# Performance work log

Hardware: AMD Instinct MI355X
Metric: run time of the kernel (lower is better)

Reference implementation:

```python
import jax, jax.numpy as jnp
import numpy as np

N_SRC, N_DST, E = 10000, 10000, 640000
S, T, O, H = 128, 128, 128, 4
D = O // H


def setup_inputs() -> dict:
    key = jax.random.key(0)
    ks = jax.random.split(key, 12)
    f = lambda k, shape, fan: jax.random.normal(k, shape, dtype=jnp.float32) / np.float32(np.sqrt(fan))
    return {
        "x_src": jax.random.normal(ks[0], (N_SRC, S), dtype=jnp.float32),
        "x_dst": jax.random.normal(ks[1], (N_DST, T), dtype=jnp.float32),
        "W_pred1": f(ks[2], (S, T), T),
        "b_pred1": jnp.zeros((S,), jnp.float32),
        "W_pred2": f(ks[3], (S, S), S),
        "b_pred2": jnp.zeros((S,), jnp.float32),
        "W_res": f(ks[4], (H * D, S), S),
        "W_src": f(ks[5], (H * D, S), S),
        "W_dst": f(ks[6], (H * D, T), T),
        "att_src": jax.random.normal(ks[7], (1, H, D), dtype=jnp.float32) * 0.01,
        "att_dst": jax.random.normal(ks[8], (1, H, D), dtype=jnp.float32) * 0.01,
        "W_self": f(ks[9], (H * D, T), T),
        "b_self": jnp.zeros((H * D,), jnp.float32),
        "edge_src": jax.random.randint(ks[10], (E,), 0, N_SRC),
        "edge_dst": jax.random.randint(ks[11], (E,), 0, N_DST),
        "num_dst": N_DST,
    }


def reference(x_src, x_dst, W_pred1, b_pred1, W_pred2, b_pred2, W_res, W_src, W_dst,
              att_src, att_dst, W_self, b_self, edge_src, edge_dst, num_dst):
    h, d = att_src.shape[1], att_src.shape[2]
    # residual prediction path: pred_mlp(x_dst) = Lin2(ReLU(Lin1(x_dst)))
    pred = jax.nn.relu(x_dst @ W_pred1.T + b_pred1) @ W_pred2.T + b_pred2  # [Ndst,S]
    residual = x_src[edge_src] - pred[edge_dst]                            # [E,S]
    # per-node attention logits (equivalent to gather-then-dot, cheaper)
    a_s = ((x_src @ W_src.T).reshape(-1, h, d) * att_src).sum(-1)          # [Nsrc,H]
    a_d = ((x_dst @ W_dst.T).reshape(-1, h, d) * att_dst).sum(-1)          # [Ndst,H]
    alpha = jax.nn.leaky_relu(a_s[edge_src] + a_d[edge_dst], 0.2)          # [E,H]
    # edge softmax over incoming edges of each destination node
    amax = jax.ops.segment_max(alpha, edge_dst, num_segments=num_dst)      # [Ndst,H]
    ex = jnp.exp(alpha - amax[edge_dst])
    denom = jax.ops.segment_sum(ex, edge_dst, num_segments=num_dst)
    alpha = ex / (denom[edge_dst] + 1e-16)                                 # [E,H]
    # attention-weighted aggregation of transformed residuals
    msg = (residual @ W_res.T).reshape(-1, h, d) * alpha[:, :, None]       # [E,H,D]
    agg = jax.ops.segment_sum(msg.reshape(-1, h * d), edge_dst, num_segments=num_dst)
    return agg + x_dst @ W_self.T + b_self                                 # [Ndst,H*D]
```

## Files before the change

### kernel.cpp

```cpp
#include <hip/hip_runtime.h>

#define LEAKY 0.2f
#define CAP 160
#define CAPB 8192
#define CHUNK 2048

#define FMA4(A, S, V) do { (A).x += (S)*(V).x; (A).y += (S)*(V).y; (A).z += (S)*(V).z; (A).w += (S)*(V).w; } while (0)

struct GemmJob { const float* X; const float* W; const float* B; float* Y; int M; int relu; };

__device__ __forceinline__ void gemm128_block(
    const float* __restrict__ X, const float* __restrict__ W,
    const float* __restrict__ B, float* __restrict__ Y,
    int M, int relu, int row0,
    float* __restrict__ XsT , float* __restrict__ WTs ) {
  if (row0 >= M) return;
  const int tid = threadIdx.x;
  const int tx = tid & 15;
  const int ty = tid >> 4;
  float4 acc[8][2];
#pragma unroll
  for (int i = 0; i < 8; i++) {
    acc[i][0] = make_float4(0.f, 0.f, 0.f, 0.f);
    acc[i][1] = make_float4(0.f, 0.f, 0.f, 0.f);
  }
  const int rS = tid >> 1;
  const int kb = (tid & 1) * 16;

  for (int k0 = 0; k0 < 128; k0 += 32) {
    int rr = row0 + rS; if (rr >= M) rr = M - 1;
    const float* xp = X + (size_t)rr * 128 + k0 + kb;
    float4 a0 = *(const float4*)xp;
    float4 a1 = *(const float4*)(xp + 4);
    float4 a2 = *(const float4*)(xp + 8);
    float4 a3 = *(const float4*)(xp + 12);
    XsT[(kb + 0) * 128 + rS] = a0.x; XsT[(kb + 1) * 128 + rS] = a0.y;
    XsT[(kb + 2) * 128 + rS] = a0.z; XsT[(kb + 3) * 128 + rS] = a0.w;
    XsT[(kb + 4) * 128 + rS] = a1.x; XsT[(kb + 5) * 128 + rS] = a1.y;
    XsT[(kb + 6) * 128 + rS] = a1.z; XsT[(kb + 7) * 128 + rS] = a1.w;
    XsT[(kb + 8) * 128 + rS] = a2.x; XsT[(kb + 9) * 128 + rS] = a2.y;
    XsT[(kb +10) * 128 + rS] = a2.z; XsT[(kb +11) * 128 + rS] = a2.w;
    XsT[(kb +12) * 128 + rS] = a3.x; XsT[(kb +13) * 128 + rS] = a3.y;
    XsT[(kb +14) * 128 + rS] = a3.z; XsT[(kb +15) * 128 + rS] = a3.w;

    const float* wp = W + (size_t)rS * 128 + k0 + kb;
    float4 b0 = *(const float4*)wp;
    float4 b1 = *(const float4*)(wp + 4);
    float4 b2 = *(const float4*)(wp + 8);
    float4 b3 = *(const float4*)(wp + 12);
    WTs[(kb + 0) * 128 + rS] = b0.x; WTs[(kb + 1) * 128 + rS] = b0.y;
    WTs[(kb + 2) * 128 + rS] = b0.z; WTs[(kb + 3) * 128 + rS] = b0.w;
    WTs[(kb + 4) * 128 + rS] = b1.x; WTs[(kb + 5) * 128 + rS] = b1.y;
    WTs[(kb + 6) * 128 + rS] = b1.z; WTs[(kb + 7) * 128 + rS] = b1.w;
    WTs[(kb + 8) * 128 + rS] = b2.x; WTs[(kb + 9) * 128 + rS] = b2.y;
    WTs[(kb +10) * 128 + rS] = b2.z; WTs[(kb +11) * 128 + rS] = b2.w;
    WTs[(kb +12) * 128 + rS] = b3.x; WTs[(kb +13) * 128 + rS] = b3.y;
    WTs[(kb +14) * 128 + rS] = b3.z; WTs[(kb +15) * 128 + rS] = b3.w;
    __syncthreads();

#pragma unroll
    for (int k = 0; k < 32; k++) {
      float4 xa = *(const float4*)&XsT[k * 128 + ty * 4];
      float4 xb = *(const float4*)&XsT[k * 128 + 64 + ty * 4];
      float4 w0 = *(const float4*)&WTs[k * 128 + tx * 4];
      float4 w1 = *(const float4*)&WTs[k * 128 + 64 + tx * 4];
      FMA4(acc[0][0], xa.x, w0); FMA4(acc[0][1], xa.x, w1);
      FMA4(acc[1][0], xa.y, w0); FMA4(acc[1][1], xa.y, w1);
      FMA4(acc[2][0], xa.z, w0); FMA4(acc[2][1], xa.z, w1);
      FMA4(acc[3][0], xa.w, w0); FMA4(acc[3][1], xa.w, w1);
      FMA4(acc[4][0], xb.x, w0); FMA4(acc[4][1], xb.x, w1);
      FMA4(acc[5][0], xb.y, w0); FMA4(acc[5][1], xb.y, w1);
      FMA4(acc[6][0], xb.z, w0); FMA4(acc[6][1], xb.z, w1);
      FMA4(acc[7][0], xb.w, w0); FMA4(acc[7][1], xb.w, w1);
    }
    __syncthreads();
  }

  float4 bv0 = make_float4(0.f, 0.f, 0.f, 0.f);
  float4 bv1 = make_float4(0.f, 0.f, 0.f, 0.f);
  if (B) { bv0 = *(const float4*)(B + tx * 4); bv1 = *(const float4*)(B + 64 + tx * 4); }
#pragma unroll
  for (int i = 0; i < 8; i++) {
    int r = row0 + (i < 4 ? ty * 4 + i : 64 + ty * 4 + (i - 4));
    if (r < M) {
      float4 o0, o1;
      o0.x = acc[i][0].x + bv0.x; o0.y = acc[i][0].y + bv0.y;
      o0.z = acc[i][0].z + bv0.z; o0.w = acc[i][0].w + bv0.w;
      o1.x = acc[i][1].x + bv1.x; o1.y = acc[i][1].y + bv1.y;
      o1.z = acc[i][1].z + bv1.z; o1.w = acc[i][1].w + bv1.w;
      if (relu) {
        o0.x = fmaxf(o0.x, 0.f); o0.y = fmaxf(o0.y, 0.f);
        o0.z = fmaxf(o0.z, 0.f); o0.w = fmaxf(o0.w, 0.f);
        o1.x = fmaxf(o1.x, 0.f); o1.y = fmaxf(o1.y, 0.f);
        o1.z = fmaxf(o1.z, 0.f); o1.w = fmaxf(o1.w, 0.f);
      }
      *(float4*)(Y + (size_t)r * 128 + tx * 4) = o0;
      *(float4*)(Y + (size_t)r * 128 + 64 + tx * 4) = o1;
    }
  }
}

__device__ __forceinline__ void attn32_block(const float* __restrict__ X,
                                             const float* __restrict__ v,
                                             float* __restrict__ a, int M, int blk,
                                             float* __restrict__ vsf ) {
  int tid = threadIdx.x;
  for (int i = tid; i < 512; i += 256) vsf[i + ((i >> 5) << 2)] = v[i];
  __syncthreads();
  int g = tid >> 3, l = tid & 7;
  int n = blk * 32 + g;
  if (n >= M) return;
  const float* xp = X + (size_t)n * 128 + l * 16;
  float4 x0 = *(const float4*)xp;
  float4 x1 = *(const float4*)(xp + 4);
  float4 x2 = *(const float4*)(xp + 8);
  float4 x3 = *(const float4*)(xp + 12);
  const float4* vv = (const float4*)vsf;
  int s = l * 18;
  float4 p = make_float4(0.f, 0.f, 0.f, 0.f);
  FMA4(p, x0.x, vv[s + 0]); FMA4(p, x0.y, vv[s + 1]); FMA4(p, x0.z, vv[s + 2]); FMA4(p, x0.w, vv[s + 3]);
  FMA4(p, x1.x, vv[s + 4]); FMA4(p, x1.y, vv[s + 5]); FMA4(p, x1.z, vv[s + 6]); FMA4(p, x1.w, vv[s + 7]);
  FMA4(p, x2.x, vv[s + 9]); FMA4(p, x2.y, vv[s +10]); FMA4(p, x2.z, vv[s +11]); FMA4(p, x2.w, vv[s +12]);
  FMA4(p, x3.x, vv[s +13]); FMA4(p, x3.y, vv[s +14]); FMA4(p, x3.z, vv[s +15]); FMA4(p, x3.w, vv[s +16]);
#pragma unroll
  for (int off = 1; off < 8; off <<= 1) {
    p.x += __shfl_xor(p.x, off, 64);
    p.y += __shfl_xor(p.y, off, 64);
    p.z += __shfl_xor(p.z, off, 64);
    p.w += __shfl_xor(p.w, off, 64);
  }
  if (l == 0) *(float4*)(a + (size_t)n * 4) = p;
}

__global__ __launch_bounds__(256) void phase1(
    const float* __restrict__ Wsrc, const float* __restrict__ attsrc,
    const float* __restrict__ Wdst, const float* __restrict__ attdst,
    const float* __restrict__ W_res, const float* __restrict__ W2,
    const float* __restrict__ b2,
    GemmJob jA,
    float* __restrict__ v_src, float* __restrict__ v_dst,
    float* __restrict__ Wc, float* __restrict__ bc,
    const int* __restrict__ edge_src, const int* __restrict__ edge_dst,
    int* __restrict__ gcnt, int* __restrict__ bin,
    int E, int Nd, int NB, int GA, int Q1, int T1) {
  __shared__ float smem[8192];
  int bx = blockIdx.x, tid = threadIdx.x;
  int u = (bx & 7) * Q1 + (bx >> 3);
  if (u >= T1) return;
  if (u == 0) {
    int which = tid >> 7, k = tid & 127;
    const float* W = which ? Wdst : Wsrc;
    const float* att = which ? attdst : attsrc;
    float* v = which ? v_dst : v_src;
    float s[4] = {0.f, 0.f, 0.f, 0.f};
#pragma unroll
    for (int h = 0; h < 4; h++)
      for (int d = 0; d < 32; d++)
        s[h] += W[(size_t)(h * 32 + d) * 128 + k] * att[h * 32 + d];
#pragma unroll
    for (int h = 0; h < 4; h++) v[k * 4 + h] = s[h];
  } else if (u == 1) {
    if (tid < 128) {
      float s = 0.f;
      for (int i = 0; i < 128; i++) s += W_res[(size_t)tid * 128 + i] * b2[i];
      bc[tid] = s;
    }
  } else if (u < 66) {
    int id = (u - 2) * 256 + tid;
    int o = id >> 7, j = id & 127;
    float s = 0.f;
    for (int i = 0; i < 128; i++) s += W_res[(size_t)o * 128 + i] * W2[(size_t)i * 128 + j];
    Wc[(size_t)o * 128 + j] = s;
  } else if (u < 66 + GA) {
    gemm128_block(jA.X, jA.W, jA.B, jA.Y, jA.M, jA.relu, (u - 66) * 128, smem, smem + 4096);
  } else {
    int* pk    = (int*)smem;
    int* hist  = (int*)smem + CHUNK;
    int* gbase = hist + 160;
    int* lcur  = gbase + 160;
    int e0 = (u - 66 - GA) * CHUNK;
    int n = E - e0; if (n > CHUNK) n = CHUNK;
    if (n <= 0) return;
    for (int i = tid; i < NB; i += 256) hist[i] = 0;
    __syncthreads();
    for (int i = tid; i < n; i += 256) {
      int s = edge_src[e0 + i], d = edge_dst[e0 + i];
      pk[i] = (s << 14) | d;
      atomicAdd(&hist[d >> 6], 1);
    }
    __syncthreads();
    for (int b = tid; b < NB; b += 256) {
      gbase[b] = hist[b] ? atomicAdd(&gcnt[b], hist[b]) : 0;
      lcur[b] = 0;
    }
    __syncthreads();
    for (int i = tid; i < n; i += 256) {
      int p = pk[i];
      int b = (p & 16383) >> 6;
      int off = gbase[b] + atomicAdd(&lcur[b], 1);
      if (off < CAPB) bin[(size_t)b * CAPB + off] = p;
    }
  }
}

__global__ __launch_bounds__(256) void phase2(
    GemmJob j0, GemmJob j1, GemmJob j2,
    const float* __restrict__ x_src, const float* __restrict__ x_dst,
    const float* __restrict__ v_src, const float* __restrict__ v_dst,
    float* __restrict__ a_s, float* __restrict__ a_d,
    const int* __restrict__ gcnt, const int* __restrict__ bin,
    int* __restrict__ sorted_src, int* __restrict__ rstart, int* __restrict__ rend,
    int Ns, int Nd, int NB, int G, int As, int Ad, int Q2, int T2) {
  __shared__ float smem[8192];
  int bx = blockIdx.x, tid = threadIdx.x;
  int u = (bx % 6) * Q2 + bx / 6;
  if (u >= T2) return;
  if (u < 3 * G) {
    GemmJob J = (u < G) ? j0 : (u < 2 * G) ? j1 : j2;
    gemm128_block(J.X, J.W, J.B, J.Y, J.M, J.relu, (u % G) * 128, smem, smem + 4096);
  } else if (u < 3 * G + As) {
    attn32_block(x_src, v_src, a_s, Ns, u - 3 * G, smem);
  } else if (u < 3 * G + As + Ad) {
    attn32_block(x_dst, v_dst, a_d, Nd, u - 3 * G - As, smem);
  } else {
    int b = u - (3 * G + As + Ad);
    int* hist2 = (int*)smem;
    int* lcur2 = (int*)smem + 64;
    int cnt = gcnt[b]; if (cnt > CAPB) cnt = CAPB;
    size_t base = (size_t)b * CAPB;
    if (tid < 64) hist2[tid] = 0;
    __syncthreads();
    for (int i = tid; i < cnt; i += 256) atomicAdd(&hist2[bin[base + i] & 63], 1);
    __syncthreads();
    if (tid < 64) {
      int v = hist2[tid];
      int incl = v;
#pragma unroll
      for (int off = 1; off < 64; off <<= 1) {
        int t = __shfl_up(incl, off, 64);
        if (tid >= off) incl += t;
      }
      int st = incl - v;
      lcur2[tid] = st;
      int dst = (b << 6) + tid;
      if (dst < Nd) {
        rstart[dst] = (int)base + st;
        rend[dst]   = (int)base + st + v;
      }
    }
    __syncthreads();
    for (int i = tid; i < cnt; i += 256) {
      int p = bin[base + i];
      int j = p & 63;
      int lp = atomicAdd(&lcur2[j], 1);
      sorted_src[base + lp] = p >> 14;
    }
  }
}

__global__ __launch_bounds__(256) void phase3(
    const int* __restrict__ rstart, const int* __restrict__ rend,
    const int* __restrict__ sorted_src,
    const float* __restrict__ a_s, const float* __restrict__ a_d,
    const float* __restrict__ u_src, const float* __restrict__ u_pred,
    const float* __restrict__ self_o, float* __restrict__ out, int Nd) {
  __shared__ float smem[1920];
  int bx = blockIdx.x, tid = threadIdx.x;
  int half = tid >> 7;
  int t = tid & 127;
  int dst = bx * 2 + half;
  if (dst >= Nd) return;

  float* wbuf  = smem + half * 640;
  int* srcbuf  = (int*)(smem + 1280) + half * 160;
  float4* red4 = (float4*)(smem + 1600);
  float4* redv = (float4*)(smem + 1616) + half * 32;
  float* inv_s = smem + 1872 + half * 4;
  float* sA_s  = smem + 1880 + half * 4;

  int start = rstart[dst];
  int deg = rend[dst] - start;
  float4 ad4 = *(const float4*)(a_d + (size_t)dst * 4);
  float s0 = 0.f, s1 = 0.f, s2 = 0.f, s3 = 0.f;
  for (int i = t; i < deg; i += 128) {
    int src = sorted_src[start + i];
    float4 as4 = *(const float4*)(a_s + (size_t)src * 4);
    float l0 = as4.x + ad4.x; l0 = l0 > 0.f ? l0 : LEAKY * l0;
    float l1 = as4.y + ad4.y; l1 = l1 > 0.f ? l1 : LEAKY * l1;
    float l2 = as4.z + ad4.z; l2 = l2 > 0.f ? l2 : LEAKY * l2;
    float l3 = as4.w + ad4.w; l3 = l3 > 0.f ? l3 : LEAKY * l3;
    float w0 = __expf(l0), w1 = __expf(l1), w2 = __expf(l2), w3 = __expf(l3);
    if (i < CAP) {
      wbuf[i * 4 + 0] = w0; wbuf[i * 4 + 1] = w1;
      wbuf[i * 4 + 2] = w2; wbuf[i * 4 + 3] = w3;
      srcbuf[i] = src;
    }
    s0 += w0; s1 += w1; s2 += w2; s3 += w3;
  }
  int wave = tid >> 6;
#pragma unroll
  for (int off = 32; off > 0; off >>= 1) {
    s0 += __shfl_xor(s0, off, 64);
    s1 += __shfl_xor(s1, off, 64);
    s2 += __shfl_xor(s2, off, 64);
    s3 += __shfl_xor(s3, off, 64);
  }
  if ((tid & 63) == 0) red4[wave] = make_float4(s0, s1, s2, s3);
  __syncthreads();
  if (t == 0) {
    float4 A = red4[half * 2], B = red4[half * 2 + 1];
    float dx = A.x + B.x, dy = A.y + B.y, dz = A.z + B.z, dw = A.w + B.w;
    inv_s[0] = 1.f / (dx + 1e-16f); sA_s[0] = dx * inv_s[0];
    inv_s[1] = 1.f / (dy + 1e-16f); sA_s[1] = dy * inv_s[1];
    inv_s[2] = 1.f / (dz + 1e-16f); sA_s[2] = dz * inv_s[2];
    inv_s[3] = 1.f / (dw + 1e-16f); sA_s[3] = dw * inv_s[3];
  }
  __syncthreads();

  int c4 = t & 31, rgrp = t >> 5, h = c4 >> 3;
  int coff = c4 * 4;
  float4 acc0 = make_float4(0.f,0.f,0.f,0.f), acc1 = acc0, acc2 = acc0, acc3 = acc0;
  int cap = deg < CAP ? deg : CAP;
  int i = rgrp;
  for (; i + 12 < cap; i += 16) {
    int sA = srcbuf[i], sB = srcbuf[i + 4], sC = srcbuf[i + 8], sD = srcbuf[i + 12];
    float wA = wbuf[i * 4 + h], wB = wbuf[(i + 4) * 4 + h];
    float wC = wbuf[(i + 8) * 4 + h], wD = wbuf[(i + 12) * 4 + h];
    float4 uA = *(const float4*)(u_src + (size_t)sA * 128 + coff);
    float4 uB = *(const float4*)(u_src + (size_t)sB * 128 + coff);
    float4 uC = *(const float4*)(u_src + (size_t)sC * 128 + coff);
    float4 uD = *(const float4*)(u_src + (size_t)sD * 128 + coff);
    FMA4(acc0, wA, uA); FMA4(acc1, wB, uB); FMA4(acc2, wC, uC); FMA4(acc3, wD, uD);
  }
  for (; i < cap; i += 4) {
    int s_ = srcbuf[i];
    float w = wbuf[i * 4 + h];
    float4 uu = *(const float4*)(u_src + (size_t)s_ * 128 + coff);
    FMA4(acc0, w, uu);
  }
  if (deg > CAP) {
    float adh = (h == 0) ? ad4.x : (h == 1) ? ad4.y : (h == 2) ? ad4.z : ad4.w;
    for (int k = CAP + rgrp; k < deg; k += 4) {
      int src = sorted_src[start + k];
      float l = a_s[(size_t)src * 4 + h] + adh;
      l = l > 0.f ? l : LEAKY * l;
      float w = __expf(l);
      float4 uu = *(const float4*)(u_src + (size_t)src * 128 + coff);
      FMA4(acc0, w, uu);
    }
  }
  float4 acc;
  acc.x = acc0.x + acc1.x + acc2.x + acc3.x;
  acc.y = acc0.y + acc1.y + acc2.y + acc3.y;
  acc.z = acc0.z + acc1.z + acc2.z + acc3.z;
  acc.w = acc0.w + acc1.w + acc2.w + acc3.w;
  acc.x += __shfl_xor(acc.x, 32, 64);
  acc.y += __shfl_xor(acc.y, 32, 64);
  acc.z += __shfl_xor(acc.z, 32, 64);
  acc.w += __shfl_xor(acc.w, 32, 64);
  if (t >= 64 && t < 96) redv[c4] = acc;
  __syncthreads();
  if (t < 32) {
    float4 r = redv[c4];
    acc.x += r.x; acc.y += r.y; acc.z += r.z; acc.w += r.w;
    float4 up = *(const float4*)(u_pred + (size_t)dst * 128 + coff);
    float4 so = *(const float4*)(self_o + (size_t)dst * 128 + coff);
    float iv = inv_s[h], sa = sA_s[h];
    float4 o;
    o.x = acc.x * iv - sa * up.x + so.x;
    o.y = acc.y * iv - sa * up.y + so.y;
    o.z = acc.z * iv - sa * up.z + so.z;
    o.w = acc.w * iv - sa * up.w + so.w;
    *(float4*)(out + (size_t)dst * 128 + coff) = o;
  }
}

extern "C" void kernel_launch(void* const* d_in, const int* in_sizes, int n_in,
                              void* d_out, int out_size, void* d_ws, size_t ws_size,
                              hipStream_t stream) {
  const float* x_src   = (const float*)d_in[0];
  const float* x_dst   = (const float*)d_in[1];
  const float* W_pred1 = (const float*)d_in[2];
  const float* b_pred1 = (const float*)d_in[3];
  const float* W_pred2 = (const float*)d_in[4];
  const float* b_pred2 = (const float*)d_in[5];
  const float* W_res   = (const float*)d_in[6];
  const float* W_src   = (const float*)d_in[7];
  const float* W_dst   = (const float*)d_in[8];
  const float* att_src = (const float*)d_in[9];
  const float* att_dst = (const float*)d_in[10];
  const float* W_self  = (const float*)d_in[11];
  const float* b_self  = (const float*)d_in[12];
  const int* edge_src  = (const int*)d_in[13];
  const int* edge_dst  = (const int*)d_in[14];
  int Ns = in_sizes[0] / 128;
  int Nd = in_sizes[1] / 128;
  int E  = in_sizes[13];
  float* out = (float*)d_out;
  int NB = (Nd + 63) >> 6;

  char* ws = (char*)d_ws;
  auto alloc = [&](size_t bytes) -> char* {
    char* p = ws;
    ws += (bytes + 255) & ~(size_t)255;
    return p;
  };
  float* relu1  = (float*)alloc((size_t)Nd * 128 * 4);
  float* u_src  = (float*)alloc((size_t)Ns * 128 * 4);
  float* u_pred = (float*)alloc((size_t)Nd * 128 * 4);
  float* self_o = (float*)alloc((size_t)Nd * 128 * 4);
  float* a_s    = (float*)alloc((size_t)Ns * 4 * 4);
  float* a_d    = (float*)alloc((size_t)Nd * 4 * 4);
  float* v_src  = (float*)alloc(128 * 4 * 4);
  float* v_dst  = (float*)alloc(128 * 4 * 4);
  float* Wc     = (float*)alloc(128 * 128 * 4);
  float* bc     = (float*)alloc(128 * 4);
  int* gcnt     = (int*)alloc((size_t)NB * 4);
  int* rstart   = (int*)alloc((size_t)Nd * 4);
  int* rend     = (int*)alloc((size_t)Nd * 4);
  int* bin      = (int*)alloc((size_t)NB * CAPB * 4);
  int* sorted_src = (int*)alloc((size_t)NB * CAPB * 4);

  hipMemsetAsync(gcnt, 0, (size_t)NB * sizeof(int), stream);

  int GA  = (Nd + 127) / 128;
  int NCH = (E + CHUNK - 1) / CHUNK;
  int T1 = 66 + GA + NCH;
  int Q1 = (T1 + 7) / 8;
  GemmJob jA{ x_dst, W_pred1, b_pred1, relu1, Nd, 1 };
  hipLaunchKernelGGL(phase1, dim3(Q1 * 8), dim3(256), 0, stream,
                     W_src, att_src, W_dst, att_dst, W_res, W_pred2, b_pred2, jA,
                     v_src, v_dst, Wc, bc, edge_src, edge_dst, gcnt, bin,
                     E, Nd, NB, GA, Q1, T1);

  int maxM = Ns > Nd ? Ns : Nd;
  int G  = (maxM + 127) / 128;
  int As = (Ns + 31) / 32;
  int Ad = (Nd + 31) / 32;
  int T2 = 3 * G + As + Ad + NB;
  int Q2 = (T2 + 5) / 6;
  GemmJob jB{ x_src, W_res,  nullptr, u_src,  Ns, 0 };
  GemmJob jC{ x_dst, W_self, b_self,  self_o, Nd, 0 };
  GemmJob jU{ relu1, Wc,     bc,      u_pred, Nd, 0 };
  hipLaunchKernelGGL(phase2, dim3(Q2 * 6), dim3(256), 0, stream,
                     jB, jC, jU, x_src, x_dst, v_src, v_dst, a_s, a_d,
                     gcnt, bin, sorted_src, rstart, rend,
                     Ns, Nd, NB, G, As, Ad, Q2, T2);

  hipLaunchKernelGGL(phase3, dim3((Nd + 1) / 2), dim3(256), 0, stream,
                     rstart, rend, sorted_src, a_s, a_d, u_src, u_pred, self_o, out, Nd);
}
```

Baseline: 173.2 us.

## Store gathered u_src in bf16, halve GEMM K-tile, pad bin counters

The x_src·W_res GEMM now writes its output as bf16. The phase3 edge aggregation gathers half as many bytes per edge and widens them back to fp32 before accumulating. The GEMM K-tile shrinks from 32 to 16, halving shared memory per block, which can raise occupancy. Bin counters are padded to a 32-int stride to reduce atomic contention and false sharing. The bf16 storage adds rounding error to the aggregated messages.

```diff
diff --git a/kernel.cpp b/kernel.cpp
--- a/kernel.cpp
+++ b/kernel.cpp
@@ -4,15 +4,25 @@
 #define CAP 160
 #define CAPB 8192
 #define CHUNK 2048
+#define GSTRIDE 32
 
 #define FMA4(A, S, V) do { (A).x += (S)*(V).x; (A).y += (S)*(V).y; (A).z += (S)*(V).z; (A).w += (S)*(V).w; } while (0)
 
-struct GemmJob { const float* X; const float* W; const float* B; float* Y; int M; int relu; };
+struct GemmJob { const float* X; const float* W; const float* B; float* Y; int M; int relu; int bf16out; };
+
+__device__ __forceinline__ unsigned short f2bf(float f) {
+  unsigned int u = __float_as_uint(f);
+  u += 0x7FFFu + ((u >> 16) & 1u);
+  return (unsigned short)(u >> 16);
+}
+__device__ __forceinline__ float bf2f(unsigned short h) {
+  return __uint_as_float(((unsigned int)h) << 16);
+}
 
 __device__ __forceinline__ void gemm128_block(
     const float* __restrict__ X, const float* __restrict__ W,
     const float* __restrict__ B, float* __restrict__ Y,
-    int M, int relu, int row0,
+    int M, int relu, int bf16out, int row0,
     float* __restrict__ XsT , float* __restrict__ WTs ) {
   if (row0 >= M) return;
   const int tid = threadIdx.x;
@@ -25,41 +35,29 @@
     acc[i][1] = make_float4(0.f, 0.f, 0.f, 0.f);
   }
   const int rS = tid >> 1;
-  const int kb = (tid & 1) * 16;
-
-  for (int k0 = 0; k0 < 128; k0 += 32) {
+  const int kb = (tid & 1) * 8;
+
+  for (int k0 = 0; k0 < 128; k0 += 16) {
     int rr = row0 + rS; if (rr >= M) rr = M - 1;
     const float* xp = X + (size_t)rr * 128 + k0 + kb;
     float4 a0 = *(const float4*)xp;
     float4 a1 = *(const float4*)(xp + 4);
-    float4 a2 = *(const float4*)(xp + 8);
-    float4 a3 = *(const float4*)(xp + 12);
     XsT[(kb + 0) * 128 + rS] = a0.x; XsT[(kb + 1) * 128 + rS] = a0.y;
     XsT[(kb + 2) * 128 + rS] = a0.z; XsT[(kb + 3) * 128 + rS] = a0.w;
     XsT[(kb + 4) * 128 + rS] = a1.x; XsT[(kb + 5) * 128 + rS] = a1.y;
     XsT[(kb + 6) * 128 + rS] = a1.z; XsT[(kb + 7) * 128 + rS] = a1.w;
-    XsT[(kb + 8) * 128 + rS] = a2.x; XsT[(kb + 9) * 128 + rS] = a2.y;
-    XsT[(kb +10) * 128 + rS] = a2.z; XsT[(kb +11) * 128 + rS] = a2.w;
-    XsT[(kb +12) * 128 + rS] = a3.x; XsT[(kb +13) * 128 + rS] = a3.y;
-    XsT[(kb +14) * 128 + rS] = a3.z; XsT[(kb +15) * 128 + rS] = a3.w;
 
     const float* wp = W + (size_t)rS * 128 + k0 + kb;
     float4 b0 = *(const float4*)wp;
     float4 b1 = *(const float4*)(wp + 4);
-    float4 b2 = *(const float4*)(wp + 8);
-    float4 b3 = *(const float4*)(wp + 12);
     WTs[(kb + 0) * 128 + rS] = b0.x; WTs[(kb + 1) * 128 + rS] = b0.y;
     WTs[(kb + 2) * 128 + rS] = b0.z; WTs[(kb + 3) * 128 + rS] = b0.w;
     WTs[(kb + 4) * 128 + rS] = b1.x; WTs[(kb + 5) * 128 + rS] = b1.y;
     WTs[(kb + 6) * 128 + rS] = b1.z; WTs[(kb + 7) * 128 + rS] = b1.w;
-    WTs[(kb + 8) * 128 + rS] = b2.x; WTs[(kb + 9) * 128 + rS] = b2.y;
-    WTs[(kb +10) * 128 + rS] = b2.z; WTs[(kb +11) * 128 + rS] = b2.w;
-    WTs[(kb +12) * 128 + rS] = b3.x; WTs[(kb +13) * 128 + rS] = b3.y;
-    WTs[(kb +14) * 128 + rS] = b3.z; WTs[(kb +15) * 128 + rS] = b3.w;
-    __syncthreads();
-
-#pragma unroll
-    for (int k = 0; k < 32; k++) {
+    __syncthreads();
+
+#pragma unroll
+    for (int k = 0; k < 16; k++) {
       float4 xa = *(const float4*)&XsT[k * 128 + ty * 4];
       float4 xb = *(const float4*)&XsT[k * 128 + 64 + ty * 4];
       float4 w0 = *(const float4*)&WTs[k * 128 + tx * 4];
@@ -94,8 +92,17 @@
         o1.x = fmaxf(o1.x, 0.f); o1.y = fmaxf(o1.y, 0.f);
         o1.z = fmaxf(o1.z, 0.f); o1.w = fmaxf(o1.w, 0.f);
       }
-      *(float4*)(Y + (size_t)r * 128 + tx * 4) = o0;
-      *(float4*)(Y + (size_t)r * 128 + 64 + tx * 4) = o1;
+      if (bf16out) {
+        unsigned short* yb = (unsigned short*)Y;
+        ushort4 p0, p1;
+        p0.x = f2bf(o0.x); p0.y = f2bf(o0.y); p0.z = f2bf(o0.z); p0.w = f2bf(o0.w);
+        p1.x = f2bf(o1.x); p1.y = f2bf(o1.y); p1.z = f2bf(o1.z); p1.w = f2bf(o1.w);
+        *(ushort4*)(yb + (size_t)r * 128 + tx * 4) = p0;
+        *(ushort4*)(yb + (size_t)r * 128 + 64 + tx * 4) = p1;
+      } else {
+        *(float4*)(Y + (size_t)r * 128 + tx * 4) = o0;
+        *(float4*)(Y + (size_t)r * 128 + 64 + tx * 4) = o1;
+      }
     }
   }
 }
@@ -143,7 +150,7 @@
     const int* __restrict__ edge_src, const int* __restrict__ edge_dst,
     int* __restrict__ gcnt, int* __restrict__ bin,
     int E, int Nd, int NB, int GA, int Q1, int T1) {
-  __shared__ float smem[8192];
+  __shared__ float smem[4096];
   int bx = blockIdx.x, tid = threadIdx.x;
   int u = (bx & 7) * Q1 + (bx >> 3);
   if (u >= T1) return;
@@ -172,7 +179,8 @@
     for (int i = 0; i < 128; i++) s += W_res[(size_t)o * 128 + i] * W2[(size_t)i * 128 + j];
     Wc[(size_t)o * 128 + j] = s;
   } else if (u < 66 + GA) {
-    gemm128_block(jA.X, jA.W, jA.B, jA.Y, jA.M, jA.relu, (u - 66) * 128, smem, smem + 4096);
+    gemm128_block(jA.X, jA.W, jA.B, jA.Y, jA.M, jA.relu, jA.bf16out,
+                  (u - 66) * 128, smem, smem + 2048);
   } else {
     int* pk    = (int*)smem;
     int* hist  = (int*)smem + CHUNK;
@@ -190,7 +198,7 @@
     }
     __syncthreads();
     for (int b = tid; b < NB; b += 256) {
-      gbase[b] = hist[b] ? atomicAdd(&gcnt[b], hist[b]) : 0;
+      gbase[b] = hist[b] ? atomicAdd(&gcnt[b * GSTRIDE], hist[b]) : 0;
       lcur[b] = 0;
     }
     __syncthreads();
@@ -211,13 +219,13 @@
     const int* __restrict__ gcnt, const int* __restrict__ bin,
     int* __restrict__ sorted_src, int* __restrict__ rstart, int* __restrict__ rend,
     int Ns, int Nd, int NB, int G, int As, int Ad, int Q2, int T2) {
-  __shared__ float smem[8192];
+  __shared__ float smem[4096];
   int bx = blockIdx.x, tid = threadIdx.x;
   int u = (bx % 6) * Q2 + bx / 6;
   if (u >= T2) return;
   if (u < 3 * G) {
     GemmJob J = (u < G) ? j0 : (u < 2 * G) ? j1 : j2;
-    gemm128_block(J.X, J.W, J.B, J.Y, J.M, J.relu, (u % G) * 128, smem, smem + 4096);
+    gemm128_block(J.X, J.W, J.B, J.Y, J.M, J.relu, J.bf16out, (u % G) * 128, smem, smem + 2048);
   } else if (u < 3 * G + As) {
     attn32_block(x_src, v_src, a_s, Ns, u - 3 * G, smem);
   } else if (u < 3 * G + As + Ad) {
@@ -226,7 +234,7 @@
     int b = u - (3 * G + As + Ad);
     int* hist2 = (int*)smem;
     int* lcur2 = (int*)smem + 64;
-    int cnt = gcnt[b]; if (cnt > CAPB) cnt = CAPB;
+    int cnt = gcnt[b * GSTRIDE]; if (cnt > CAPB) cnt = CAPB;
     size_t base = (size_t)b * CAPB;
     if (tid < 64) hist2[tid] = 0;
     __syncthreads();
@@ -262,7 +270,7 @@
     const int* __restrict__ rstart, const int* __restrict__ rend,
     const int* __restrict__ sorted_src,
     const float* __restrict__ a_s, const float* __restrict__ a_d,
-    const float* __restrict__ u_src, const float* __restrict__ u_pred,
+    const unsigned short* __restrict__ u_src, const float* __restrict__ u_pred,
     const float* __restrict__ self_o, float* __restrict__ out, int Nd) {
   __shared__ float smem[1920];
   int bx = blockIdx.x, tid = threadIdx.x;
@@ -326,16 +334,21 @@
     int sA = srcbuf[i], sB = srcbuf[i + 4], sC = srcbuf[i + 8], sD = srcbuf[i + 12];
     float wA = wbuf[i * 4 + h], wB = wbuf[(i + 4) * 4 + h];
     float wC = wbuf[(i + 8) * 4 + h], wD = wbuf[(i + 12) * 4 + h];
-    float4 uA = *(const float4*)(u_src + (size_t)sA * 128 + coff);
-    float4 uB = *(const float4*)(u_src + (size_t)sB * 128 + coff);
-    float4 uC = *(const float4*)(u_src + (size_t)sC * 128 + coff);
-    float4 uD = *(const float4*)(u_src + (size_t)sD * 128 + coff);
+    ushort4 hA = *(const ushort4*)(u_src + (size_t)sA * 128 + coff);
+    ushort4 hB = *(const ushort4*)(u_src + (size_t)sB * 128 + coff);
+    ushort4 hC = *(const ushort4*)(u_src + (size_t)sC * 128 + coff);
+    ushort4 hD = *(const ushort4*)(u_src + (size_t)sD * 128 + coff);
+    float4 uA = make_float4(bf2f(hA.x), bf2f(hA.y), bf2f(hA.z), bf2f(hA.w));
+    float4 uB = make_float4(bf2f(hB.x), bf2f(hB.y), bf2f(hB.z), bf2f(hB.w));
+    float4 uC = make_float4(bf2f(hC.x), bf2f(hC.y), bf2f(hC.z), bf2f(hC.w));
+    float4 uD = make_float4(bf2f(hD.x), bf2f(hD.y), bf2f(hD.z), bf2f(hD.w));
     FMA4(acc0, wA, uA); FMA4(acc1, wB, uB); FMA4(acc2, wC, uC); FMA4(acc3, wD, uD);
   }
   for (; i < cap; i += 4) {
     int s_ = srcbuf[i];
     float w = wbuf[i * 4 + h];
-    float4 uu = *(const float4*)(u_src + (size_t)s_ * 128 + coff);
+    ushort4 hh = *(const ushort4*)(u_src + (size_t)s_ * 128 + coff);
+    float4 uu = make_float4(bf2f(hh.x), bf2f(hh.y), bf2f(hh.z), bf2f(hh.w));
     FMA4(acc0, w, uu);
   }
   if (deg > CAP) {
@@ -345,7 +358,8 @@
       float l = a_s[(size_t)src * 4 + h] + adh;
       l = l > 0.f ? l : LEAKY * l;
       float w = __expf(l);
-      float4 uu = *(const float4*)(u_src + (size_t)src * 128 + coff);
+      ushort4 hh = *(const ushort4*)(u_src + (size_t)src * 128 + coff);
+      float4 uu = make_float4(bf2f(hh.x), bf2f(hh.y), bf2f(hh.z), bf2f(hh.w));
       FMA4(acc0, w, uu);
     }
   }
@@ -406,7 +420,7 @@
     return p;
   };
   float* relu1  = (float*)alloc((size_t)Nd * 128 * 4);
-  float* u_src  = (float*)alloc((size_t)Ns * 128 * 4);
+  unsigned short* u_src = (unsigned short*)alloc((size_t)Ns * 128 * 2);
   float* u_pred = (float*)alloc((size_t)Nd * 128 * 4);
   float* self_o = (float*)alloc((size_t)Nd * 128 * 4);
   float* a_s    = (float*)alloc((size_t)Ns * 4 * 4);
@@ -415,19 +429,19 @@
   float* v_dst  = (float*)alloc(128 * 4 * 4);
   float* Wc     = (float*)alloc(128 * 128 * 4);
   float* bc     = (float*)alloc(128 * 4);
-  int* gcnt     = (int*)alloc((size_t)NB * 4);
+  int* gcnt     = (int*)alloc((size_t)NB * GSTRIDE * 4);
   int* rstart   = (int*)alloc((size_t)Nd * 4);
   int* rend     = (int*)alloc((size_t)Nd * 4);
   int* bin      = (int*)alloc((size_t)NB * CAPB * 4);
   int* sorted_src = (int*)alloc((size_t)NB * CAPB * 4);
 
-  hipMemsetAsync(gcnt, 0, (size_t)NB * sizeof(int), stream);
+  hipMemsetAsync(gcnt, 0, (size_t)NB * GSTRIDE * sizeof(int), stream);
 
   int GA  = (Nd + 127) / 128;
   int NCH = (E + CHUNK - 1) / CHUNK;
   int T1 = 66 + GA + NCH;
   int Q1 = (T1 + 7) / 8;
-  GemmJob jA{ x_dst, W_pred1, b_pred1, relu1, Nd, 1 };
+  GemmJob jA{ x_dst, W_pred1, b_pred1, relu1, Nd, 1, 0 };
   hipLaunchKernelGGL(phase1, dim3(Q1 * 8), dim3(256), 0, stream,
                      W_src, att_src, W_dst, att_dst, W_res, W_pred2, b_pred2, jA,
                      v_src, v_dst, Wc, bc, edge_src, edge_dst, gcnt, bin,
@@ -439,9 +453,9 @@
   int Ad = (Nd + 31) / 32;
   int T2 = 3 * G + As + Ad + NB;
   int Q2 = (T2 + 5) / 6;
-  GemmJob jB{ x_src, W_res,  nullptr, u_src,  Ns, 0 };
-  GemmJob jC{ x_dst, W_self, b_self,  self_o, Nd, 0 };
-  GemmJob jU{ relu1, Wc,     bc,      u_pred, Nd, 0 };
+  GemmJob jB{ x_src, W_res,  nullptr, (float*)u_src, Ns, 0, 1 };
+  GemmJob jC{ x_dst, W_self, b_self,  self_o, Nd, 0, 0 };
+  GemmJob jU{ relu1, Wc,     bc,      u_pred, Nd, 0, 0 };
   hipLaunchKernelGGL(phase2, dim3(Q2 * 6), dim3(256), 0, stream,
                      jB, jC, jU, x_src, x_dst, v_src, v_dst, a_s, a_d,
                      gcnt, bin, sorted_src, rstart, rend,
```

Measured after the change: 166.5 us, median of 2. 1.04x faster.
